# Optimization experiments

Hardware: AMD Instinct MI355X
Metric: run time of the kernel (lower is better)

## Reference

```python
import jax, jax.numpy as jnp
import numpy as np

N_NODES = 100000
N_EDGES = 3200000
IN_F = 256
OUT_F = 256


def setup_inputs() -> dict:
    key = jax.random.key(0)
    k1, k2, k3, k4, k5 = jax.random.split(key, 5)
    input_ = jax.random.normal(k1, (N_NODES, IN_F), dtype=jnp.float32)
    edge_src = jax.random.randint(k2, (N_EDGES,), 0, N_NODES, dtype=jnp.int64)
    edge_dst = jax.random.randint(k3, (N_EDGES,), 0, N_NODES, dtype=jnp.int64)
    edge_val = jax.random.uniform(k4, (N_EDGES,), dtype=jnp.float32)
    stdv = 1.0 / np.sqrt(OUT_F)
    weight = jax.random.uniform(k5, (IN_F, OUT_F), dtype=jnp.float32,
                                minval=-stdv, maxval=stdv)
    return {"input_": input_, "edge_src": edge_src, "edge_dst": edge_dst,
            "edge_val": edge_val, "weight": weight}


def reference(input_, edge_src, edge_dst, edge_val, weight):
    # neighbor = spmm(adj, input_): adj in COO form (dst, src, val)
    gathered = edge_val[:, None] * input_[edge_src]          # [E, F]
    neighbor = jax.ops.segment_sum(gathered, edge_dst,
                                   num_segments=N_NODES)     # [N, F]
    ft_input = input_ @ weight                               # [N, O]
    ft_neighbor = neighbor @ weight                          # [N, O]
    return jnp.concatenate([ft_input, ft_neighbor], axis=1)  # [N, 2*O]
```

## Files before the change

kernel.cpp:

```cpp
#include <hip/hip_runtime.h>

#define N_NODES 100000
#define N_EDGES 3200000
#define F 256

#define BM 128
#define BN 128
#define BK 32

#define SCAN_NB ((N_NODES + 255) / 256)
#define EDGE_NB (N_EDGES / 256)

typedef __attribute__((ext_vector_type(8))) short short8;
typedef __attribute__((ext_vector_type(4))) float f32x4;

__device__ inline unsigned short f2bf(float f) {
    unsigned int u = __float_as_uint(f);
    unsigned int r = (u + 0x7fffu + ((u >> 16) & 1u)) >> 16;
    return (unsigned short)r;
}

__device__ inline float bf2f(unsigned short b) {
    return __uint_as_float(((unsigned int)b) << 16);
}

__global__ void wt_kernel(const float* __restrict__ W, unsigned short* __restrict__ Wt) {
    int idx = blockIdx.x * 256 + threadIdx.x;
    int n = idx >> 8;
    int k = idx & 255;
    Wt[n * 256 + k] = f2bf(W[k * 256 + n]);
}

__global__ __launch_bounds__(256)
void rank_hist_kernel(const int* __restrict__ dst, int* __restrict__ counts,
                      unsigned short* __restrict__ rank) {
    const int e = blockIdx.x * 256 + threadIdx.x;
    rank[e] = (unsigned short)atomicAdd(&counts[dst[e]], 1);
}

__global__ __launch_bounds__(256)
void scan1_kernel(const int* __restrict__ counts, int* __restrict__ row_start,
                  int* __restrict__ partials) {
    __shared__ int s[256];
    const int t = threadIdx.x;
    const int i = blockIdx.x * 256 + t;
    int v = (i < N_NODES) ? counts[i] : 0;
    s[t] = v;
    __syncthreads();
#pragma unroll
    for (int off = 1; off < 256; off <<= 1) {
        int x = (t >= off) ? s[t - off] : 0;
        __syncthreads();
        if (t >= off) s[t] += x;
        __syncthreads();
    }
    if (i < N_NODES) row_start[i] = s[t] - v;
    if (t == 255) partials[blockIdx.x] = s[t];
}

__global__ __launch_bounds__(512)
void scan2_kernel(int* __restrict__ partials) {
    __shared__ int s[512];
    const int t = threadIdx.x;
    int v = (t < SCAN_NB) ? partials[t] : 0;
    s[t] = v;
    __syncthreads();
#pragma unroll
    for (int off = 1; off < 512; off <<= 1) {
        int x = (t >= off) ? s[t - off] : 0;
        __syncthreads();
        if (t >= off) s[t] += x;
        __syncthreads();
    }
    if (t < SCAN_NB) partials[t] = s[t] - v;
}

__global__ __launch_bounds__(256)
void scan3_kernel(int* __restrict__ row_start, const int* __restrict__ partials) {
    const int i = blockIdx.x * 256 + threadIdx.x;
    if (i < N_NODES)
        row_start[i] += partials[blockIdx.x];
    if (i == 0) row_start[N_NODES] = N_EDGES;
}

__global__ __launch_bounds__(256)
void fill_kernel(const int* __restrict__ src, const int* __restrict__ dst,
                 const float* __restrict__ val,
                 const int* __restrict__ row_start,
                 const unsigned short* __restrict__ rank,
                 int2* __restrict__ recs) {
    const int e = blockIdx.x * 256 + threadIdx.x;
    const int d = dst[e];
    const int pos = row_start[d] + (int)rank[e];
    recs[pos] = make_int2(src[e], __float_as_int(val[e]));
}

__global__ __launch_bounds__(256, 2)
void gemm_kernel(const float* __restrict__ A,
                 const unsigned short* __restrict__ Wt,
                 float* __restrict__ out,
                 unsigned short* __restrict__ ftb)
{
    __shared__ unsigned short As[BM * BK];
    __shared__ unsigned short Bs[BN * BK];

    const int tid   = threadIdx.x;
    const int lane  = tid & 63;
    const int wave  = tid >> 6;
    const int waveM = wave >> 1;
    const int waveN = wave & 1;
    const int rowBase = blockIdx.x * BM;
    const int bn      = blockIdx.y;

    f32x4 acc[4][4];
#pragma unroll
    for (int i = 0; i < 4; i++)
#pragma unroll
        for (int j = 0; j < 4; j++) acc[i][j] = (f32x4)0.0f;

    const int sr = tid >> 2;
    const int sk = (tid & 3) * 8;
    const int quad = lane >> 4;
    const int l16  = lane & 15;

    for (int kt = 0; kt < 8; kt++) {
        const int k0 = kt * BK;
#pragma unroll
        for (int p = 0; p < 2; p++) {
            const int r = p * 64 + sr;
            const int grow = rowBase + r;
            short8 av;
            if (grow < N_NODES) {
                const float4* pa = (const float4*)(A + (size_t)grow * 256 + k0 + sk);
                float4 f0 = pa[0];
                float4 f1 = pa[1];
                av[0] = (short)f2bf(f0.x); av[1] = (short)f2bf(f0.y);
                av[2] = (short)f2bf(f0.z); av[3] = (short)f2bf(f0.w);
                av[4] = (short)f2bf(f1.x); av[5] = (short)f2bf(f1.y);
                av[6] = (short)f2bf(f1.z); av[7] = (short)f2bf(f1.w);
            } else {
                av = (short8)0;
            }
            *(short8*)(&As[r * BK + sk]) = av;

            const uint4 wv = *(const uint4*)(Wt + (size_t)(bn * BN + r) * 256 + k0 + sk);
            *(uint4*)(&Bs[r * BK + sk]) = wv;
        }
        __syncthreads();

        short8 af[4], bfr[4];
#pragma unroll
        for (int i = 0; i < 4; i++)
            af[i] = *(const short8*)(&As[(waveM * 64 + i * 16 + l16) * BK + quad * 8]);
#pragma unroll
        for (int j = 0; j < 4; j++)
            bfr[j] = *(const short8*)(&Bs[(waveN * 64 + j * 16 + l16) * BK + quad * 8]);
#pragma unroll
        for (int i = 0; i < 4; i++)
#pragma unroll
            for (int j = 0; j < 4; j++)
                acc[i][j] = __builtin_amdgcn_mfma_f32_16x16x32_bf16(
                    af[i], bfr[j], acc[i][j], 0, 0, 0);
        __syncthreads();
    }

    const int colBase = bn * BN + waveN * 64;
#pragma unroll
    for (int i = 0; i < 4; i++) {
        const int row0 = rowBase + waveM * 64 + i * 16 + quad * 4;
#pragma unroll
        for (int j = 0; j < 4; j++) {
            const int col = colBase + j * 16 + l16;
#pragma unroll
            for (int r = 0; r < 4; r++) {
                const int row = row0 + r;
                if (row < N_NODES) {
                    float v = acc[i][j][r];
                    out[(size_t)row * 512 + col] = v;
                    ftb[(size_t)row * 256 + col] = f2bf(v);
                }
            }
        }
    }
}

__global__ __launch_bounds__(256)
void gather_kernel(const int* __restrict__ row_start,
                   const int2* __restrict__ recs,
                   const unsigned short* __restrict__ ftb,
                   float* __restrict__ out)
{
    const int n = blockIdx.x * 4 + (threadIdx.x >> 6);
    if (n >= N_NODES) return;
    const int lane = threadIdx.x & 63;

    const int beg = row_start[n];
    const int end = row_start[n + 1];

    float ax = 0.f, ay = 0.f, az = 0.f, aw = 0.f;

    int e = beg;
    for (; e + 3 < end; e += 4) {
        int2 r0 = recs[e];
        int2 r1 = recs[e + 1];
        int2 r2 = recs[e + 2];
        int2 r3 = recs[e + 3];
        ushort4 u0 = *(const ushort4*)(ftb + (size_t)r0.x * 256 + lane * 4);
        ushort4 u1 = *(const ushort4*)(ftb + (size_t)r1.x * 256 + lane * 4);
        ushort4 u2 = *(const ushort4*)(ftb + (size_t)r2.x * 256 + lane * 4);
        ushort4 u3 = *(const ushort4*)(ftb + (size_t)r3.x * 256 + lane * 4);
        const float v0 = __int_as_float(r0.y);
        const float v1 = __int_as_float(r1.y);
        const float v2 = __int_as_float(r2.y);
        const float v3 = __int_as_float(r3.y);
        ax += v0 * bf2f(u0.x); ay += v0 * bf2f(u0.y);
        az += v0 * bf2f(u0.z); aw += v0 * bf2f(u0.w);
        ax += v1 * bf2f(u1.x); ay += v1 * bf2f(u1.y);
        az += v1 * bf2f(u1.z); aw += v1 * bf2f(u1.w);
        ax += v2 * bf2f(u2.x); ay += v2 * bf2f(u2.y);
        az += v2 * bf2f(u2.z); aw += v2 * bf2f(u2.w);
        ax += v3 * bf2f(u3.x); ay += v3 * bf2f(u3.y);
        az += v3 * bf2f(u3.z); aw += v3 * bf2f(u3.w);
    }
    for (; e < end; e++) {
        int2 r0 = recs[e];
        ushort4 u0 = *(const ushort4*)(ftb + (size_t)r0.x * 256 + lane * 4);
        const float v0 = __int_as_float(r0.y);
        ax += v0 * bf2f(u0.x); ay += v0 * bf2f(u0.y);
        az += v0 * bf2f(u0.z); aw += v0 * bf2f(u0.w);
    }

    float4 res = make_float4(ax, ay, az, aw);
    *(float4*)(out + (size_t)n * 512 + 256 + lane * 4) = res;
}

extern "C" void kernel_launch(void* const* d_in, const int* in_sizes, int n_in,
                              void* d_out, int out_size, void* d_ws, size_t ws_size,
                              hipStream_t stream)
{
    const float* input = (const float*)d_in[0];
    const int*   esrc  = (const int*)d_in[1];
    const int*   edst  = (const int*)d_in[2];
    const float* eval  = (const float*)d_in[3];
    const float* W     = (const float*)d_in[4];
    float* out = (float*)d_out;

    char* ws = (char*)d_ws;
    unsigned short* Wt   = (unsigned short*)(ws);
    int* counts          = (int*)(ws + 131072);
    int* row_start       = (int*)(ws + 532480);
    unsigned short* rank = (unsigned short*)(ws + 933888);
    int* partials        = (int*)(ws + 7334912);
    int2* recs           = (int2*)(ws + 7337984);
    unsigned short* ftb  = (unsigned short*)(ws + 7337984 + (size_t)N_EDGES * 8);

    hipMemsetAsync(counts, 0, N_NODES * sizeof(int), stream);

    wt_kernel<<<256, 256, 0, stream>>>(W, Wt);
    rank_hist_kernel<<<EDGE_NB, 256, 0, stream>>>(edst, counts, rank);
    scan1_kernel<<<SCAN_NB, 256, 0, stream>>>(counts, row_start, partials);
    scan2_kernel<<<1, 512, 0, stream>>>(partials);
    scan3_kernel<<<SCAN_NB, 256, 0, stream>>>(row_start, partials);
    fill_kernel<<<EDGE_NB, 256, 0, stream>>>(esrc, edst, eval, row_start, rank, recs);

    dim3 g((N_NODES + BM - 1) / BM, 2);
    gemm_kernel<<<g, 256, 0, stream>>>(input, Wt, out, ftb);

    gather_kernel<<<(N_NODES + 3) / 4, 256, 0, stream>>>(row_start, recs, ftb, out);
}
```

Before: 772.3 us.

## Widen GEMM tile to full output width and prefetch edge records in gather

The GEMM now covers all 256 output columns per block (BN 256, single grid dimension), so each input row tile is loaded and converted to bf16 once instead of twice. This doubles the accumulator registers per wave (32 f32x4) and the B shared-memory tile, which may reduce occupancy. The gather kernel adds an 8-edge unrolled loop that prefetches the next batch of edge records while the current batch of feature rows is loaded, to increase memory-level parallelism at the cost of more registers.

Result: faster. 743.7 us (-3.7%).

```diff
diff --git a/kernel.cpp b/kernel.cpp
--- a/kernel.cpp
+++ b/kernel.cpp
@@ -5,7 +5,7 @@
 #define F 256
 
 #define BM 128
-#define BN 128
+#define BN 256
 #define BK 32
 
 #define SCAN_NB ((N_NODES + 255) / 256)
@@ -110,13 +110,12 @@
     const int waveM = wave >> 1;
     const int waveN = wave & 1;
     const int rowBase = blockIdx.x * BM;
-    const int bn      = blockIdx.y;
-
-    f32x4 acc[4][4];
+
+    f32x4 acc[4][8];
 #pragma unroll
     for (int i = 0; i < 4; i++)
 #pragma unroll
-        for (int j = 0; j < 4; j++) acc[i][j] = (f32x4)0.0f;
+        for (int j = 0; j < 8; j++) acc[i][j] = (f32x4)0.0f;
 
     const int sr = tid >> 2;
     const int sk = (tid & 3) * 8;
@@ -142,34 +141,37 @@
                 av = (short8)0;
             }
             *(short8*)(&As[r * BK + sk]) = av;
-
-            const uint4 wv = *(const uint4*)(Wt + (size_t)(bn * BN + r) * 256 + k0 + sk);
+        }
+#pragma unroll
+        for (int p = 0; p < 4; p++) {
+            const int r = p * 64 + sr;
+            const uint4 wv = *(const uint4*)(Wt + (size_t)r * 256 + k0 + sk);
             *(uint4*)(&Bs[r * BK + sk]) = wv;
         }
         __syncthreads();
 
-        short8 af[4], bfr[4];
+        short8 af[4], bfr[8];
 #pragma unroll
         for (int i = 0; i < 4; i++)
             af[i] = *(const short8*)(&As[(waveM * 64 + i * 16 + l16) * BK + quad * 8]);
 #pragma unroll
-        for (int j = 0; j < 4; j++)
-            bfr[j] = *(const short8*)(&Bs[(waveN * 64 + j * 16 + l16) * BK + quad * 8]);
+        for (int j = 0; j < 8; j++)
+            bfr[j] = *(const short8*)(&Bs[(waveN * 128 + j * 16 + l16) * BK + quad * 8]);
 #pragma unroll
         for (int i = 0; i < 4; i++)
 #pragma unroll
-            for (int j = 0; j < 4; j++)
+            for (int j = 0; j < 8; j++)
                 acc[i][j] = __builtin_amdgcn_mfma_f32_16x16x32_bf16(
                     af[i], bfr[j], acc[i][j], 0, 0, 0);
         __syncthreads();
     }
 
-    const int colBase = bn * BN + waveN * 64;
+    const int colBase = waveN * 128;
 #pragma unroll
     for (int i = 0; i < 4; i++) {
         const int row0 = rowBase + waveM * 64 + i * 16 + quad * 4;
 #pragma unroll
-        for (int j = 0; j < 4; j++) {
+        for (int j = 0; j < 8; j++) {
             const int col = colBase + j * 16 + l16;
 #pragma unroll
             for (int r = 0; r < 4; r++) {
@@ -200,6 +202,36 @@
     float ax = 0.f, ay = 0.f, az = 0.f, aw = 0.f;
 
     int e = beg;
+
+    if (e + 7 < end) {
+        int2 r[8];
+#pragma unroll
+        for (int q = 0; q < 8; q++) r[q] = recs[e + q];
+        while (true) {
+            const int en = e + 8;
+            const bool moreN = (en + 7 < end);
+            int2 rn[8];
+            if (moreN) {
+#pragma unroll
+                for (int q = 0; q < 8; q++) rn[q] = recs[en + q];
+            }
+            ushort4 u[8];
+#pragma unroll
+            for (int q = 0; q < 8; q++)
+                u[q] = *(const ushort4*)(ftb + (size_t)r[q].x * 256 + lane * 4);
+#pragma unroll
+            for (int q = 0; q < 8; q++) {
+                const float v = __int_as_float(r[q].y);
+                ax += v * bf2f(u[q].x); ay += v * bf2f(u[q].y);
+                az += v * bf2f(u[q].z); aw += v * bf2f(u[q].w);
+            }
+            e = en;
+            if (!moreN) break;
+#pragma unroll
+            for (int q = 0; q < 8; q++) r[q] = rn[q];
+        }
+    }
+
     for (; e + 3 < end; e += 4) {
         int2 r0 = recs[e];
         int2 r1 = recs[e + 1];
@@ -263,7 +295,7 @@
     scan3_kernel<<<SCAN_NB, 256, 0, stream>>>(row_start, partials);
     fill_kernel<<<EDGE_NB, 256, 0, stream>>>(esrc, edst, eval, row_start, rank, recs);
 
-    dim3 g((N_NODES + BM - 1) / BM, 2);
+    dim3 g((N_NODES + BM - 1) / BM);
     gemm_kernel<<<g, 256, 0, stream>>>(input, Wt, out, ftb);
 
     gather_kernel<<<(N_NODES + 3) / 4, 256, 0, stream>>>(row_start, recs, ftb, out);
```
